# Performance work log

Hardware: AMD Instinct MI355X
Metric: run time of the kernel (lower is better)

## Reference

```python
import jax, jax.numpy as jnp
import numpy as np

E = 11        # number of language experts
ALPHA = 1000.0  # soft-argmax temperature
C1 = 8.0      # gate sharpness


def setup_inputs() -> dict:
    key = jax.random.key(0)
    ks = jax.random.split(key, 6)
    B, S, H, L = 16, 256, 1024, 32
    return {
        "transformer_out": jax.random.normal(ks[0], (B, S, H), dtype=jnp.float32),
        "logits_ld": jax.random.normal(ks[1], (B, E), dtype=jnp.float32),
        "W1": jax.random.normal(ks[2], (E, H, H), dtype=jnp.float32) * 0.02,
        "b1": jax.random.normal(ks[3], (E, H), dtype=jnp.float32) * 0.02,
        "W2": jax.random.normal(ks[4], (E, H, L), dtype=jnp.float32) * 0.02,
        "b2": jax.random.normal(ks[5], (E, L), dtype=jnp.float32) * 0.02,
    }


def reference(transformer_out, logits_ld, W1, b1, W2, b2):
    # soft argmax over language-detect logits -> continuous lang id per sample [B]
    sm = jax.nn.softmax(logits_ld * ALPHA, axis=1)
    lang_id = jnp.sum(sm * jnp.arange(logits_ld.shape[1], dtype=logits_ld.dtype), axis=1)

    # soft top-hat gate per expert i: sigmoid((id-(i-.5))*c1)*sigmoid(((i+.5)-id)*c1) -> [E,B]
    idx = jnp.arange(E, dtype=lang_id.dtype)[:, None]          # [E,1]
    gate = (jax.nn.sigmoid((lang_id[None, :] - (idx - 0.5)) * C1)
            * jax.nn.sigmoid((idx + 0.5 - lang_id[None, :]) * C1))  # [E,B]

    # all 11 expert FFN branches as batched GEMMs (dropout = identity in eval)
    h = jax.nn.relu(jnp.einsum('bsh,ehd->ebsd', transformer_out, W1)
                    + b1[:, None, None, :])                     # [E,B,S,H]
    t = jnp.einsum('ebsd,edl->ebsl', h, W2) + b2[:, None, None, :]  # [E,B,S,L]

    # gate per (expert, batch) and sum over experts -> [B,S,L]
    logits = jnp.einsum('ebsl,eb->bsl', t, gate)
    return logits
```

## Files before the change

kernel.cpp:

```cpp
#include <hip/hip_runtime.h>
#include <hip/hip_bf16.h>
#include <stdint.h>

#define E_ 11
#define B_ 16
#define S_ 256
#define H_ 1024
#define L_ 32
#define GEPS 1e-4f

typedef __attribute__((ext_vector_type(8))) short short8;
typedef __attribute__((ext_vector_type(4))) float f32x4;

__device__ __forceinline__ unsigned short f2bf(float f) {
  unsigned u = __float_as_uint(f);
  unsigned r = (u + 0x7FFFu + ((u >> 16) & 1u)) >> 16;
  return (unsigned short)r;
}
__device__ __forceinline__ float bf2f(unsigned short v) {
  return __uint_as_float(((unsigned)v) << 16);
}
__device__ __forceinline__ void gload_lds16(const void* g, void* l) {
  __builtin_amdgcn_global_load_lds(
      (const __attribute__((address_space(1))) unsigned int*)g,
      (__attribute__((address_space(3))) unsigned int*)l, 16, 0, 0);
}
__device__ __forceinline__ float sigf(float x) { return 1.0f / (1.0f + expf(-x)); }

__device__ __forceinline__ float lang_of(const float* __restrict__ logits, int b) {
  float lv[E_];
  float m = -1e30f;
  #pragma unroll
  for (int i = 0; i < E_; ++i) { lv[i] = logits[b * E_ + i]; m = fmaxf(m, lv[i]); }
  float den = 0.f, num = 0.f;
  #pragma unroll
  for (int i = 0; i < E_; ++i) {
    float z = expf((lv[i] - m) * 1000.0f);
    den += z; num += z * (float)i;
  }
  return num / den;
}

__device__ __forceinline__ bool expert_active(const float* __restrict__ logits, int e) {
  int b = threadIdx.x & 15;
  float lang = lang_of(logits, b);
  unsigned long long m = __ballot(fabsf(lang - (float)e) < 1.7f);
  return m != 0ull;
}

__global__ __launch_bounds__(256) void prep_kernel(
    const float* __restrict__ x, const float* __restrict__ logits,
    const float* __restrict__ W1, const float* __restrict__ W2,
    unsigned short* __restrict__ xbf, unsigned short* __restrict__ W1T,
    unsigned short* __restrict__ W2T) {
  int bid = blockIdx.x;
  int tid = threadIdx.x;
  __shared__ float t[64][65];

  if (bid < 2048) {
    int i = (bid * 256 + tid) * 8;
    float4 f0 = *(const float4*)(x + i);
    float4 f1 = *(const float4*)(x + i + 4);
    short8 o;
    o[0] = (short)f2bf(f0.x); o[1] = (short)f2bf(f0.y);
    o[2] = (short)f2bf(f0.z); o[3] = (short)f2bf(f0.w);
    o[4] = (short)f2bf(f1.x); o[5] = (short)f2bf(f1.y);
    o[6] = (short)f2bf(f1.z); o[7] = (short)f2bf(f1.w);
    *(short8*)(xbf + i) = o;
    return;
  }
  if (bid < 2048 + 2816) {
    int tt = bid - 2048;
    int e = tt >> 8, rest = tt & 255;
    int k0 = (rest >> 4) * 64, d0 = (rest & 15) * 64;
    if (!expert_active(logits, e)) return;
    int kr = tid >> 2, dc = (tid & 3) * 16;
    const float* src = W1 + ((size_t)e << 20) + (size_t)(k0 + kr) * H_ + d0 + dc;
    #pragma unroll
    for (int q = 0; q < 4; ++q) {
      float4 v = *(const float4*)(src + q * 4);
      t[kr][dc + q * 4 + 0] = v.x; t[kr][dc + q * 4 + 1] = v.y;
      t[kr][dc + q * 4 + 2] = v.z; t[kr][dc + q * 4 + 3] = v.w;
    }
    __syncthreads();
    int dr = tid >> 2, kc = (tid & 3) * 16;
    short8 v0, v1;
    #pragma unroll
    for (int j = 0; j < 8; ++j) v0[j] = (short)f2bf(t[kc + j][dr]);
    #pragma unroll
    for (int j = 0; j < 8; ++j) v1[j] = (short)f2bf(t[kc + 8 + j][dr]);
    unsigned short* dst = W1T + ((size_t)e << 20) + (size_t)(d0 + dr) * H_ + k0 + kc;
    *(short8*)(dst) = v0;
    *(short8*)(dst + 8) = v1;
    return;
  }
  {
    int tt = bid - 4864;
    int e = tt >> 4, k0 = (tt & 15) * 64;
    if (!expert_active(logits, e)) return;
    int kr = tid >> 2, lc = (tid & 3) * 8;
    const float* src = W2 + (size_t)e * H_ * L_ + (size_t)(k0 + kr) * L_ + lc;
    float4 a = *(const float4*)(src);
    float4 b = *(const float4*)(src + 4);
    t[kr][lc + 0] = a.x; t[kr][lc + 1] = a.y; t[kr][lc + 2] = a.z; t[kr][lc + 3] = a.w;
    t[kr][lc + 4] = b.x; t[kr][lc + 5] = b.y; t[kr][lc + 6] = b.z; t[kr][lc + 7] = b.w;
    __syncthreads();
    int lr = tid >> 3, kc = (tid & 7) * 8;
    short8 v;
    #pragma unroll
    for (int j = 0; j < 8; ++j) v[j] = (short)f2bf(t[kc + j][lr]);
    *(short8*)(W2T + (size_t)(e * L_ + lr) * H_ + k0 + kc) = v;
  }
}

#define WAITV(N) asm volatile("s_waitcnt vmcnt(" #N ")" ::: "memory")

__global__ __launch_bounds__(512, 4) void ffn_kernel(
    const unsigned short* __restrict__ xbf, const unsigned short* __restrict__ W1T,
    const unsigned short* __restrict__ W2T, const float* __restrict__ b1,
    const float* __restrict__ b2, const float* __restrict__ logits,
    float* __restrict__ out) {
  int bid = blockIdx.x;
  int r8 = bid & 7, gq = bid >> 3;
  int sblk = gq & 1, uq = gq >> 1;
  int u = uq * 8 + r8;
  int pair = u >> 2, dt = u & 3;
  int e = pair >> 4, b = pair & 15;
  int s0 = sblk * 128;
  float lang = lang_of(logits, b);
  float fe = (float)e;
  float g = sigf((lang - (fe - 0.5f)) * 8.0f) * sigf(((fe + 0.5f) - lang) * 8.0f);
  if (g < GEPS) return;

  __shared__ __align__(16) char smem[73728];

  int tid = threadIdx.x;
  int w = tid >> 6, wr = w >> 2, wc = w & 3;
  int l = tid & 63;
  int l15 = l & 15, l4 = l >> 4;

  int pA = tid >> 3, slA = tid & 7, uA = slA ^ (pA & 7);
  const unsigned short* gA =
      xbf + (size_t)(b * S_ + s0 + pA * 2 + (uA >> 2)) * H_ + (uA & 3) * 8;
  int ldsA = tid * 16;
  const unsigned short* gB[2];
  int ldsB[2];
  #pragma unroll
  for (int jj = 0; jj < 2; ++jj) {
    int c = jj * 512 + tid;
    int p = c >> 3, slot = c & 7, uu = slot ^ (p & 7);
    gB[jj] = W1T + ((size_t)e * H_ + dt * 256 + p * 2 + (uu >> 2)) * H_ + (uu & 3) * 8;
    ldsB[jj] = 8192 + c * 16;
  }
  int offA[4], offB[4];
  #pragma unroll
  for (int mf = 0; mf < 4; ++mf) {
    int row = wr * 64 + mf * 16 + l15;
    int p = row >> 1;
    int slot = (((row & 1) * 4) + l4) ^ (p & 7);
    offA[mf] = p * 128 + slot * 16;
  }
  #pragma unroll
  for (int nf = 0; nf < 4; ++nf) {
    int d = wc * 64 + nf * 16 + l15;
    int p = d >> 1;
    int slot = (((d & 1) * 4) + l4) ^ (p & 7);
    offB[nf] = 8192 + p * 128 + slot * 16;
  }

  f32x4 acc[4][4];
  #pragma unroll
  for (int mf = 0; mf < 4; ++mf)
    #pragma unroll
    for (int nf = 0; nf < 4; ++nf) acc[mf][nf] = f32x4{0.f, 0.f, 0.f, 0.f};

  auto stage = [&](int buf, int kt) {
    int bb = buf * 24576;
    int ko = kt * 32;
    gload_lds16(gA + ko, smem + bb + ldsA);
    gload_lds16(gB[0] + ko, smem + bb + ldsB[0]);
    gload_lds16(gB[1] + ko, smem + bb + ldsB[1]);
  };

  stage(0, 0);
  stage(1, 1);

  #pragma unroll
  for (int kt = 0; kt < 32; ++kt) {
    __builtin_amdgcn_s_barrier();
    if (kt < 30) {
      stage((kt + 2) % 3, kt + 2);
      WAITV(6);
    } else if (kt == 30) {
      WAITV(3);
    } else {
      WAITV(0);
    }
    __builtin_amdgcn_s_barrier();
    int bb = (kt % 3) * 24576;
    short8 af[4], bf[4];
    #pragma unroll
    for (int mf = 0; mf < 4; ++mf) af[mf] = *(const short8*)(smem + bb + offA[mf]);
    #pragma unroll
    for (int nf = 0; nf < 4; ++nf) bf[nf] = *(const short8*)(smem + bb + offB[nf]);
    asm volatile("s_waitcnt lgkmcnt(0)" ::: "memory");
    __builtin_amdgcn_sched_barrier(0);
    __builtin_amdgcn_s_setprio(1);
    #pragma unroll
    for (int mf = 0; mf < 4; ++mf)
      #pragma unroll
      for (int nf = 0; nf < 4; ++nf)
        acc[mf][nf] =
            __builtin_amdgcn_mfma_f32_16x16x32_bf16(af[mf], bf[nf], acc[mf][nf], 0, 0, 0);
    __builtin_amdgcn_s_setprio(0);
  }

  __syncthreads();

  float b1v[4];
  #pragma unroll
  for (int nf = 0; nf < 4; ++nf)
    b1v[nf] = b1[e * H_ + dt * 256 + wc * 64 + nf * 16 + l15];

  char* P = smem + w * 8192;
  #pragma unroll
  for (int mf = 0; mf < 4; ++mf)
    #pragma unroll
    for (int nf = 0; nf < 4; ++nf)
      #pragma unroll
      for (int rr = 0; rr < 4; ++rr) {
        int row = mf * 16 + l4 * 4 + rr;
        int col = nf * 16 + l15;
        float v = fmaxf(acc[mf][nf][rr] + b1v[nf], 0.f);
        *(unsigned short*)(P + row * 128 + (((col >> 3) ^ (row & 7)) * 16) +
                           (col & 7) * 2) = f2bf(v);
      }
  asm volatile("s_waitcnt lgkmcnt(0)" ::: "memory");

  f32x4 tacc[4][2];
  #pragma unroll
  for (int mf = 0; mf < 4; ++mf)
    #pragma unroll
    for (int nl = 0; nl < 2; ++nl) tacc[mf][nl] = f32x4{0.f, 0.f, 0.f, 0.f};
  #pragma unroll
  for (int kk = 0; kk < 2; ++kk) {
    short8 ap[4], bw[2];
    #pragma unroll
    for (int mf = 0; mf < 4; ++mf) {
      int row = mf * 16 + l15;
      int ch = kk * 4 + l4;
      ap[mf] = *(const short8*)(P + row * 128 + ((ch ^ (row & 7)) * 16));
    }
    #pragma unroll
    for (int nl = 0; nl < 2; ++nl)
      bw[nl] = *(const short8*)(W2T + (size_t)(e * L_ + nl * 16 + l15) * H_ +
                                dt * 256 + wc * 64 + kk * 32 + l4 * 8);
    #pragma unroll
    for (int mf = 0; mf < 4; ++mf)
      #pragma unroll
      for (int nl = 0; nl < 2; ++nl)
        tacc[mf][nl] =
            __builtin_amdgcn_mfma_f32_16x16x32_bf16(ap[mf], bw[nl], tacc[mf][nl], 0, 0, 0);
  }

  float* Tr = (float*)smem + w * 2048;
  #pragma unroll
  for (int mf = 0; mf < 4; ++mf)
    #pragma unroll
    for (int nl = 0; nl < 2; ++nl)
      #pragma unroll
      for (int rr = 0; rr < 4; ++rr) {
        int row = mf * 16 + l4 * 4 + rr;
        int col = nl * 16 + l15;
        Tr[row * 32 + col] = tacc[mf][nl][rr];
      }
  __syncthreads();
  float* Tb = (float*)smem;
  #pragma unroll
  for (int jj = 0; jj < 8; ++jj) {
    int ei = tid + jj * 512;
    int srow = ei >> 5, lcol = ei & 31;
    int wr2 = srow >> 6, r6 = srow & 63;
    float sum = Tb[(wr2 * 4 + 0) * 2048 + r6 * 32 + lcol] +
                Tb[(wr2 * 4 + 1) * 2048 + r6 * 32 + lcol] +
                Tb[(wr2 * 4 + 2) * 2048 + r6 * 32 + lcol] +
                Tb[(wr2 * 4 + 3) * 2048 + r6 * 32 + lcol];
    if (dt == 0) sum += b2[e * L_ + lcol];
    atomicAdd(out + (size_t)(b * S_ + s0 + srow) * L_ + lcol, g * sum);
  }
}

__global__ void fb_kernel(const float* __restrict__ x, const float* __restrict__ logits,
                          const float* __restrict__ W1, const float* __restrict__ b1,
                          const float* __restrict__ W2, const float* __restrict__ b2,
                          float* __restrict__ out) {
  int bid = blockIdx.x;
  int e = bid >> 9;
  int r = bid & 511;
  int b = r >> 5, st = r & 31, s0 = st * 8;
  float lang = lang_of(logits, b);
  float fe = (float)e;
  float g = sigf((lang - (fe - 0.5f)) * 8.0f) * sigf(((fe + 0.5f) - lang) * 8.0f);
  if (g < GEPS) return;

  __shared__ float xs[8][H_];
  __shared__ unsigned short hs[8][H_];
  int tid = threadIdx.x;
  for (int jj = 0; jj < 32; ++jj) {
    int idx = tid + jj * 256;
    int s = idx >> 10, k = idx & 1023;
    xs[s][k] = x[(size_t)(b * S_ + s0 + s) * H_ + k];
  }
  __syncthreads();
  for (int qq = 0; qq < 4; ++qq) {
    int d = tid + qq * 256;
    float a[8];
    #pragma unroll
    for (int s = 0; s < 8; ++s) a[s] = 0.f;
    for (int k = 0; k < H_; ++k) {
      float wv = W1[((size_t)e << 20) + (size_t)k * H_ + d];
      #pragma unroll
      for (int s = 0; s < 8; ++s) a[s] += xs[s][k] * wv;
    }
    float bv = b1[e * H_ + d];
    #pragma unroll
    for (int s = 0; s < 8; ++s) hs[s][d] = f2bf(fmaxf(a[s] + bv, 0.f));
  }
  __syncthreads();
  int s = tid >> 5, lcol = tid & 31;
  float acc = 0.f;
  for (int d = 0; d < H_; ++d)
    acc += bf2f(hs[s][d]) * W2[(size_t)(e * H_ + d) * L_ + lcol];
  acc += b2[e * L_ + lcol];
  atomicAdd(out + (size_t)(b * S_ + s0 + s) * L_ + lcol, g * acc);
}

extern "C" void kernel_launch(void* const* d_in, const int* in_sizes, int n_in,
                              void* d_out, int out_size, void* d_ws, size_t ws_size,
                              hipStream_t stream) {
  (void)in_sizes; (void)n_in;
  const float* x  = (const float*)d_in[0];
  const float* lg = (const float*)d_in[1];
  const float* W1 = (const float*)d_in[2];
  const float* b1 = (const float*)d_in[3];
  const float* W2 = (const float*)d_in[4];
  const float* b2 = (const float*)d_in[5];
  float* out = (float*)d_out;

  hipMemsetAsync(d_out, 0, (size_t)out_size * sizeof(float), stream);

  const size_t OFF_X = 0;
  const size_t OFF_W1 = OFF_X + 8388608;
  const size_t OFF_W2 = OFF_W1 + 23068672;
  const size_t WS_NEED = OFF_W2 + 720896;

  if (ws_size >= WS_NEED) {
    unsigned short* xbf = (unsigned short*)((char*)d_ws + OFF_X);
    unsigned short* W1T = (unsigned short*)((char*)d_ws + OFF_W1);
    unsigned short* W2T = (unsigned short*)((char*)d_ws + OFF_W2);
    prep_kernel<<<2048 + 2816 + 176, 256, 0, stream>>>(x, lg, W1, W2, xbf, W1T, W2T);
    ffn_kernel<<<8 * 88 * 2, 512, 0, stream>>>(xbf, W1T, W2T, b1, b2, lg, out);
  } else {
    fb_kernel<<<E_ * B_ * (S_ / 8), 256, 0, stream>>>(x, lg, W1, b1, W2, b2, out);
  }
}
```

Before: 66.31 us.

## Compact active expert-batch pairs into a plan and enlarge FFN tiles

The prep kernel gains an extra block that computes the gates and writes a compacted list of active (expert, batch) pairs to the workspace. The FFN kernel then launches only as many useful blocks as there are active pairs, instead of launching every pair and exiting early. Each block now covers all 256 sequence rows with a 256x256 tile (8 N-fragments per wave, 96KB LDS, launch bounds lowered to 2 blocks per CU). This raises data reuse and removes idle blocks, but increases register and LDS pressure and leaves fewer blocks to run in parallel.

```diff
diff --git a/kernel.cpp b/kernel.cpp
--- a/kernel.cpp
+++ b/kernel.cpp
@@ -40,6 +40,10 @@
   }
   return num / den;
 }
+__device__ __forceinline__ float gate_of(float lang, int e) {
+  float fe = (float)e;
+  return sigf((lang - (fe - 0.5f)) * 8.0f) * sigf(((fe + 0.5f) - lang) * 8.0f);
+}
 
 __device__ __forceinline__ bool expert_active(const float* __restrict__ logits, int e) {
   int b = threadIdx.x & 15;
@@ -52,7 +56,7 @@
     const float* __restrict__ x, const float* __restrict__ logits,
     const float* __restrict__ W1, const float* __restrict__ W2,
     unsigned short* __restrict__ xbf, unsigned short* __restrict__ W1T,
-    unsigned short* __restrict__ W2T) {
+    unsigned short* __restrict__ W2T, int* __restrict__ plan) {
   int bid = blockIdx.x;
   int tid = threadIdx.x;
   __shared__ float t[64][65];
@@ -94,7 +98,7 @@
     *(short8*)(dst + 8) = v1;
     return;
   }
-  {
+  if (bid < 2048 + 2816 + 176) {
     int tt = bid - 4864;
     int e = tt >> 4, k0 = (tt & 15) * 64;
     if (!expert_active(logits, e)) return;
@@ -110,49 +114,64 @@
     #pragma unroll
     for (int j = 0; j < 8; ++j) v[j] = (short)f2bf(t[kc + j][lr]);
     *(short8*)(W2T + (size_t)(e * L_ + lr) * H_ + k0 + kc) = v;
+    return;
+  }
+  {
+    __shared__ float langs[16];
+    __shared__ int wcnt[4];
+    if (tid < 16) langs[tid] = lang_of(logits, tid);
+    __syncthreads();
+    bool act = false;
+    if (tid < E_ * B_) {
+      int e = tid >> 4, b = tid & 15;
+      act = gate_of(langs[b], e) >= GEPS;
+    }
+    unsigned long long m = __ballot(act);
+    int w = tid >> 6;
+    if ((tid & 63) == 0) wcnt[w] = __popcll(m);
+    __syncthreads();
+    int off = 0;
+    for (int i = 0; i < w; ++i) off += wcnt[i];
+    int rank = __popcll(m & ((1ull << (tid & 63)) - 1ull));
+    if (act) plan[1 + off + rank] = tid;
+    if (tid == 0) plan[0] = wcnt[0] + wcnt[1] + wcnt[2] + wcnt[3];
   }
 }
 
 #define WAITV(N) asm volatile("s_waitcnt vmcnt(" #N ")" ::: "memory")
 
-__global__ __launch_bounds__(512, 4) void ffn_kernel(
+__global__ __launch_bounds__(512, 2) void ffn_kernel(
     const unsigned short* __restrict__ xbf, const unsigned short* __restrict__ W1T,
     const unsigned short* __restrict__ W2T, const float* __restrict__ b1,
     const float* __restrict__ b2, const float* __restrict__ logits,
-    float* __restrict__ out) {
+    const int* __restrict__ plan, float* __restrict__ out) {
   int bid = blockIdx.x;
-  int r8 = bid & 7, gq = bid >> 3;
-  int sblk = gq & 1, uq = gq >> 1;
-  int u = uq * 8 + r8;
-  int pair = u >> 2, dt = u & 3;
+  int cnt = plan[0];
+  if (bid >= (cnt << 2)) return;
+  int pair = plan[1 + (bid >> 2)];
+  int dt = bid & 3;
   int e = pair >> 4, b = pair & 15;
-  int s0 = sblk * 128;
-  float lang = lang_of(logits, b);
-  float fe = (float)e;
-  float g = sigf((lang - (fe - 0.5f)) * 8.0f) * sigf(((fe + 0.5f) - lang) * 8.0f);
-  if (g < GEPS) return;
-
-  __shared__ __align__(16) char smem[73728];
+  float g = gate_of(lang_of(logits, b), e);
+
+  __shared__ __align__(16) char smem[98304];
 
   int tid = threadIdx.x;
-  int w = tid >> 6, wr = w >> 2, wc = w & 3;
-  int l = tid & 63;
-  int l15 = l & 15, l4 = l >> 4;
-
-  int pA = tid >> 3, slA = tid & 7, uA = slA ^ (pA & 7);
-  const unsigned short* gA =
-      xbf + (size_t)(b * S_ + s0 + pA * 2 + (uA >> 2)) * H_ + (uA & 3) * 8;
-  int ldsA = tid * 16;
-  const unsigned short* gB[2];
-  int ldsB[2];
+  int w = tid >> 6, wr = w >> 1, wc = w & 1;
+  int l = tid & 63, l15 = l & 15, l4 = l >> 4;
+
+  const unsigned short* gA[2]; int ldsA[2];
+  const unsigned short* gB[2]; int ldsB[2];
   #pragma unroll
   for (int jj = 0; jj < 2; ++jj) {
     int c = jj * 512 + tid;
-    int p = c >> 3, slot = c & 7, uu = slot ^ (p & 7);
-    gB[jj] = W1T + ((size_t)e * H_ + dt * 256 + p * 2 + (uu >> 2)) * H_ + (uu & 3) * 8;
-    ldsB[jj] = 8192 + c * 16;
-  }
-  int offA[4], offB[4];
+    int p = c >> 3, uu = (c & 7) ^ (p & 7);
+    int row = p * 2 + (uu >> 2), kc = (uu & 3) * 8;
+    gA[jj] = xbf + (size_t)(b * S_ + row) * H_ + kc;
+    ldsA[jj] = c * 16;
+    gB[jj] = W1T + ((size_t)e * H_ + dt * 256 + row) * H_ + kc;
+    ldsB[jj] = 16384 + c * 16;
+  }
+  int offA[4], offB[8];
   #pragma unroll
   for (int mf = 0; mf < 4; ++mf) {
     int row = wr * 64 + mf * 16 + l15;
@@ -161,23 +180,24 @@
     offA[mf] = p * 128 + slot * 16;
   }
   #pragma unroll
-  for (int nf = 0; nf < 4; ++nf) {
-    int d = wc * 64 + nf * 16 + l15;
+  for (int nf = 0; nf < 8; ++nf) {
+    int d = wc * 128 + nf * 16 + l15;
     int p = d >> 1;
     int slot = (((d & 1) * 4) + l4) ^ (p & 7);
-    offB[nf] = 8192 + p * 128 + slot * 16;
-  }
-
-  f32x4 acc[4][4];
+    offB[nf] = 16384 + p * 128 + slot * 16;
+  }
+
+  f32x4 acc[4][8];
   #pragma unroll
   for (int mf = 0; mf < 4; ++mf)
     #pragma unroll
-    for (int nf = 0; nf < 4; ++nf) acc[mf][nf] = f32x4{0.f, 0.f, 0.f, 0.f};
+    for (int nf = 0; nf < 8; ++nf) acc[mf][nf] = f32x4{0.f, 0.f, 0.f, 0.f};
 
   auto stage = [&](int buf, int kt) {
-    int bb = buf * 24576;
+    int bb = buf * 32768;
     int ko = kt * 32;
-    gload_lds16(gA + ko, smem + bb + ldsA);
+    gload_lds16(gA[0] + ko, smem + bb + ldsA[0]);
+    gload_lds16(gA[1] + ko, smem + bb + ldsA[1]);
     gload_lds16(gB[0] + ko, smem + bb + ldsB[0]);
     gload_lds16(gB[1] + ko, smem + bb + ldsB[1]);
   };
@@ -190,26 +210,26 @@
     __builtin_amdgcn_s_barrier();
     if (kt < 30) {
       stage((kt + 2) % 3, kt + 2);
-      WAITV(6);
+      WAITV(8);
     } else if (kt == 30) {
-      WAITV(3);
+      WAITV(4);
     } else {
       WAITV(0);
     }
     __builtin_amdgcn_s_barrier();
-    int bb = (kt % 3) * 24576;
-    short8 af[4], bf[4];
+    int bb = (kt % 3) * 32768;
+    short8 af[4], bf[8];
     #pragma unroll
     for (int mf = 0; mf < 4; ++mf) af[mf] = *(const short8*)(smem + bb + offA[mf]);
     #pragma unroll
-    for (int nf = 0; nf < 4; ++nf) bf[nf] = *(const short8*)(smem + bb + offB[nf]);
+    for (int nf = 0; nf < 8; ++nf) bf[nf] = *(const short8*)(smem + bb + offB[nf]);
     asm volatile("s_waitcnt lgkmcnt(0)" ::: "memory");
     __builtin_amdgcn_sched_barrier(0);
     __builtin_amdgcn_s_setprio(1);
     #pragma unroll
     for (int mf = 0; mf < 4; ++mf)
       #pragma unroll
-      for (int nf = 0; nf < 4; ++nf)
+      for (int nf = 0; nf < 8; ++nf)
         acc[mf][nf] =
             __builtin_amdgcn_mfma_f32_16x16x32_bf16(af[mf], bf[nf], acc[mf][nf], 0, 0, 0);
     __builtin_amdgcn_s_setprio(0);
@@ -217,50 +237,56 @@
 
   __syncthreads();
 
-  float b1v[4];
-  #pragma unroll
-  for (int nf = 0; nf < 4; ++nf)
-    b1v[nf] = b1[e * H_ + dt * 256 + wc * 64 + nf * 16 + l15];
+  float b1v[8];
+  #pragma unroll
+  for (int nf = 0; nf < 8; ++nf)
+    b1v[nf] = b1[e * H_ + dt * 256 + wc * 128 + nf * 16 + l15];
 
   char* P = smem + w * 8192;
+  f32x4 tacc[4][2];
   #pragma unroll
   for (int mf = 0; mf < 4; ++mf)
     #pragma unroll
-    for (int nf = 0; nf < 4; ++nf)
-      #pragma unroll
-      for (int rr = 0; rr < 4; ++rr) {
-        int row = mf * 16 + l4 * 4 + rr;
-        int col = nf * 16 + l15;
-        float v = fmaxf(acc[mf][nf][rr] + b1v[nf], 0.f);
-        *(unsigned short*)(P + row * 128 + (((col >> 3) ^ (row & 7)) * 16) +
-                           (col & 7) * 2) = f2bf(v);
+    for (int nl = 0; nl < 2; ++nl) tacc[mf][nl] = f32x4{0.f, 0.f, 0.f, 0.f};
+
+  #pragma unroll
+  for (int half = 0; half < 2; ++half) {
+    #pragma unroll
+    for (int mf = 0; mf < 4; ++mf)
+      #pragma unroll
+      for (int nfh = 0; nfh < 4; ++nfh) {
+        int nf = half * 4 + nfh;
+        #pragma unroll
+        for (int rr = 0; rr < 4; ++rr) {
+          int row = mf * 16 + l4 * 4 + rr;
+          int col = nfh * 16 + l15;
+          float v = fmaxf(acc[mf][nf][rr] + b1v[nf], 0.f);
+          *(unsigned short*)(P + row * 128 + (((col >> 3) ^ (row & 7)) * 16) +
+                             (col & 7) * 2) = f2bf(v);
+        }
       }
-  asm volatile("s_waitcnt lgkmcnt(0)" ::: "memory");
-
-  f32x4 tacc[4][2];
-  #pragma unroll
-  for (int mf = 0; mf < 4; ++mf)
-    #pragma unroll
-    for (int nl = 0; nl < 2; ++nl) tacc[mf][nl] = f32x4{0.f, 0.f, 0.f, 0.f};
-  #pragma unroll
-  for (int kk = 0; kk < 2; ++kk) {
-    short8 ap[4], bw[2];
-    #pragma unroll
-    for (int mf = 0; mf < 4; ++mf) {
-      int row = mf * 16 + l15;
-      int ch = kk * 4 + l4;
-      ap[mf] = *(const short8*)(P + row * 128 + ((ch ^ (row & 7)) * 16));
-    }
-    #pragma unroll
-    for (int nl = 0; nl < 2; ++nl)
-      bw[nl] = *(const short8*)(W2T + (size_t)(e * L_ + nl * 16 + l15) * H_ +
-                                dt * 256 + wc * 64 + kk * 32 + l4 * 8);
-    #pragma unroll
-    for (int mf = 0; mf < 4; ++mf)
+    asm volatile("s_waitcnt lgkmcnt(0)" ::: "memory");
+    #pragma unroll
+    for (int kk = 0; kk < 2; ++kk) {
+      short8 ap[4], bw[2];
+      #pragma unroll
+      for (int mf = 0; mf < 4; ++mf) {
+        int row = mf * 16 + l15;
+        int ch = kk * 4 + l4;
+        ap[mf] = *(const short8*)(P + row * 128 + ((ch ^ (row & 7)) * 16));
+      }
       #pragma unroll
       for (int nl = 0; nl < 2; ++nl)
-        tacc[mf][nl] =
-            __builtin_amdgcn_mfma_f32_16x16x32_bf16(ap[mf], bw[nl], tacc[mf][nl], 0, 0, 0);
+        bw[nl] = *(const short8*)(W2T + (size_t)(e * L_ + nl * 16 + l15) * H_ +
+                                  dt * 256 + wc * 128 + half * 64 + kk * 32 + l4 * 8);
+      #pragma unroll
+      for (int mf = 0; mf < 4; ++mf)
+        #pragma unroll
+        for (int nl = 0; nl < 2; ++nl)
+          tacc[mf][nl] =
+              __builtin_amdgcn_mfma_f32_16x16x32_bf16(ap[mf], bw[nl], tacc[mf][nl], 0, 0, 0);
+    }
+    asm volatile("s_waitcnt lgkmcnt(0)" ::: "memory");
   }
 
   float* Tr = (float*)smem + w * 2048;
@@ -277,16 +303,14 @@
   __syncthreads();
   float* Tb = (float*)smem;
   #pragma unroll
-  for (int jj = 0; jj < 8; ++jj) {
+  for (int jj = 0; jj < 16; ++jj) {
     int ei = tid + jj * 512;
     int srow = ei >> 5, lcol = ei & 31;
     int wr2 = srow >> 6, r6 = srow & 63;
-    float sum = Tb[(wr2 * 4 + 0) * 2048 + r6 * 32 + lcol] +
-                Tb[(wr2 * 4 + 1) * 2048 + r6 * 32 + lcol] +
-                Tb[(wr2 * 4 + 2) * 2048 + r6 * 32 + lcol] +
-                Tb[(wr2 * 4 + 3) * 2048 + r6 * 32 + lcol];
+    float sum = Tb[(wr2 * 2 + 0) * 2048 + r6 * 32 + lcol] +
+                Tb[(wr2 * 2 + 1) * 2048 + r6 * 32 + lcol];
     if (dt == 0) sum += b2[e * L_ + lcol];
-    atomicAdd(out + (size_t)(b * S_ + s0 + srow) * L_ + lcol, g * sum);
+    atomicAdd(out + (size_t)(b * S_ + srow) * L_ + lcol, g * sum);
   }
 }
 
@@ -298,9 +322,7 @@
   int e = bid >> 9;
   int r = bid & 511;
   int b = r >> 5, st = r & 31, s0 = st * 8;
-  float lang = lang_of(logits, b);
-  float fe = (float)e;
-  float g = sigf((lang - (fe - 0.5f)) * 8.0f) * sigf(((fe + 0.5f) - lang) * 8.0f);
+  float g = gate_of(lang_of(logits, b), e);
   if (g < GEPS) return;
 
   __shared__ float xs[8][H_];
@@ -352,14 +374,16 @@
   const size_t OFF_X = 0;
   const size_t OFF_W1 = OFF_X + 8388608;
   const size_t OFF_W2 = OFF_W1 + 23068672;
-  const size_t WS_NEED = OFF_W2 + 720896;
+  const size_t OFF_PLAN = OFF_W2 + 720896;
+  const size_t WS_NEED = OFF_PLAN + 1024;
 
   if (ws_size >= WS_NEED) {
     unsigned short* xbf = (unsigned short*)((char*)d_ws + OFF_X);
     unsigned short* W1T = (unsigned short*)((char*)d_ws + OFF_W1);
     unsigned short* W2T = (unsigned short*)((char*)d_ws + OFF_W2);
-    prep_kernel<<<2048 + 2816 + 176, 256, 0, stream>>>(x, lg, W1, W2, xbf, W1T, W2T);
-    ffn_kernel<<<8 * 88 * 2, 512, 0, stream>>>(xbf, W1T, W2T, b1, b2, lg, out);
+    int* plan = (int*)((char*)d_ws + OFF_PLAN);
+    prep_kernel<<<2048 + 2816 + 176 + 1, 256, 0, stream>>>(x, lg, W1, W2, xbf, W1T, W2T, plan);
+    ffn_kernel<<<704, 512, 0, stream>>>(xbf, W1T, W2T, b1, b2, lg, plan, out);
   } else {
     fb_kernel<<<E_ * B_ * (S_ / 8), 256, 0, stream>>>(x, lg, W1, b1, W2, b2, out);
   }
```

New measurement: 65.09 us. Within noise of the previous version (-1.8%).
